# Optimization experiments

Measured on AMD Instinct MI355X. Metric: run time of the kernel, lower is better.

The kernel has to match this reference:

```python
import jax, jax.numpy as jnp
import numpy as np

N_NODES = 50000
NEG_SLOPE = 0.2  # PyG GATConv default LeakyReLU slope


def gat_conv(x, src, dst, W, att_src, att_dst, bias, heads, out_ch, concat):
    """PyG-style GATConv (dropout=0, add_self_loops omitted to match raw edge list usage).
    x: [N, in], W: [in, heads*out_ch], att_*: [1, heads, out_ch], bias: [heads*out_ch] or [out_ch].
    Messages flow src -> dst; softmax normalizes over incoming edges of each dst node."""
    N = x.shape[0]
    h = (x @ W).reshape(N, heads, out_ch)                      # [N,H,C]
    a_s = (h * att_src).sum(-1)                                # [N,H]
    a_d = (h * att_dst).sum(-1)                                # [N,H]
    e = jax.nn.leaky_relu(a_s[src] + a_d[dst], NEG_SLOPE)      # [E,H] per-edge logits
    m = jax.ops.segment_max(e, dst, num_segments=N)            # [N,H] stable softmax max
    p = jnp.exp(e - m[dst])                                    # [E,H]
    s = jax.ops.segment_sum(p, dst, num_segments=N)            # [N,H]
    alpha = p / (s[dst] + 1e-16)                               # [E,H] attention coeffs
    out = jax.ops.segment_sum(h[src] * alpha[:, :, None], dst, num_segments=N)  # [N,H,C]
    out = out.reshape(N, heads * out_ch) if concat else out.mean(axis=1)
    return out + bias


def setup_inputs() -> dict:
    key = jax.random.key(0)
    ks = jax.random.split(key, 10)
    in_ch, hid, heads, out_ch = 128, 32, 4, 64
    E = 800000
    x = jax.random.normal(ks[0], (N_NODES, in_ch), dtype=jnp.float32)
    edge_index = jax.random.randint(ks[1], (2, E), 0, N_NODES, dtype=jnp.int64)
    sc = 0.1
    return {
        "x": x,
        "edge_index": edge_index,
        "W1": jax.random.normal(ks[2], (in_ch, heads * hid), dtype=jnp.float32) * sc,
        "att_src1": jax.random.normal(ks[3], (1, heads, hid), dtype=jnp.float32) * sc,
        "att_dst1": jax.random.normal(ks[4], (1, heads, hid), dtype=jnp.float32) * sc,
        "b1": jnp.zeros((heads * hid,), dtype=jnp.float32),
        "W2": jax.random.normal(ks[5], (heads * hid, out_ch), dtype=jnp.float32) * sc,
        "att_src2": jax.random.normal(ks[6], (1, 1, out_ch), dtype=jnp.float32) * sc,
        "att_dst2": jax.random.normal(ks[7], (1, 1, out_ch), dtype=jnp.float32) * sc,
        "b2": jnp.zeros((out_ch,), dtype=jnp.float32),
    }


def reference(x, edge_index, W1, att_src1, att_dst1, b1, W2, att_src2, att_dst2, b2):
    src, dst = edge_index[0], edge_index[1]
    h = gat_conv(x, src, dst, W1, att_src1, att_dst1, b1, heads=4, out_ch=32, concat=True)
    h = jax.nn.elu(h)
    out = gat_conv(h, src, dst, W2, att_src2, att_dst2, b2, heads=1, out_ch=64, concat=False)
    return out
```

## Files before the change

kernel.cpp:

```cpp
#include <hip/hip_runtime.h>

#define N_NODES 50000
#define N_EDGES 800000
#define GEMM_BLKS ((N_NODES + 63) / 64)
#define FILL_BLKS 4096
#define RANGE 6250
#define EDGES_PER_BLK 1564
#define MAXDEG 64
#define AGG_BLKS (N_NODES / 4)

typedef __attribute__((ext_vector_type(8))) short bf16x8;
typedef __attribute__((ext_vector_type(4))) float f32x4;
typedef unsigned short u16;
typedef unsigned int u32;

__device__ __forceinline__ float lrelu(float x) { return x > 0.f ? x : 0.2f * x; }

__device__ __forceinline__ u16 f2bf(float f) {
    u32 u = __float_as_uint(f);
    return (u16)((u + 0x7FFFu + ((u >> 16) & 1u)) >> 16);
}
__device__ __forceinline__ float bflo(u32 w) { return __uint_as_float(w << 16); }
__device__ __forceinline__ float bfhi(u32 w) { return __uint_as_float(w & 0xFFFF0000u); }
__device__ __forceinline__ float elu(float x) { return x > 0.f ? x : __expf(x) - 1.f; }

__global__ __launch_bounds__(256) void k_prep(
    const float* __restrict__ W1, const float* __restrict__ as1v, const float* __restrict__ ad1v,
    const float* __restrict__ W2, const float* __restrict__ as2v, const float* __restrict__ ad2v,
    u16* __restrict__ Wt1, u16* __restrict__ Wt2, int* __restrict__ deg)
{
    int gid = blockIdx.x * 256 + threadIdx.x;
    for (int i = gid; i < N_NODES; i += 112 * 256) deg[i] = 0;
    if (gid < 144 * 128) {
        int n = gid >> 7, k = gid & 127;
        float v = 0.f;
        if (n < 128) v = W1[k * 128 + n];
        else if (n < 136) {
            int h = n - 128;
            const float* att = (h < 4) ? as1v : ad1v;
            int hh = h & 3;
            float s = 0.f;
            for (int c = 0; c < 32; ++c) s += W1[k * 128 + hh * 32 + c] * att[hh * 32 + c];
            v = s;
        }
        Wt1[n * 128 + k] = f2bf(v);
    } else {
        int g2 = gid - 144 * 128;
        if (g2 < 80 * 128) {
            int n = g2 >> 7, k = g2 & 127;
            float v = 0.f;
            if (n < 64) v = W2[k * 64 + n];
            else if (n == 64) { float s = 0.f; for (int c = 0; c < 64; ++c) s += W2[k * 64 + c] * as2v[c]; v = s; }
            else if (n == 65) { float s = 0.f; for (int c = 0; c < 64; ++c) s += W2[k * 64 + c] * ad2v[c]; v = s; }
            Wt2[n * 128 + k] = f2bf(v);
        }
    }
}

__global__ __launch_bounds__(256) void k_fill(
    const int* __restrict__ src, const int* __restrict__ dst,
    int* __restrict__ deg, u16* __restrict__ col16)
{
    const int g = blockIdx.x & 7;
    const int b = blockIdx.x >> 3;
    const int lo = g * RANGE;
    const int hi = min(lo + RANGE, N_NODES);
    const int e0 = b * EDGES_PER_BLK;
    const int e1 = min(e0 + EDGES_PER_BLK, N_EDGES);
    for (int e = e0 + threadIdx.x; e < e1; e += 256) {
        int v = dst[e];
        if (v >= lo && v < hi) {
            int pos = atomicAdd(&deg[v], 1);
            if (pos < MAXDEG) col16[v * MAXDEG + pos] = (u16)src[e];
        }
    }
}

__global__ __launch_bounds__(256) void k_gemm1(
    const float* __restrict__ x, const u16* __restrict__ Wt1,
    u16* __restrict__ hbf, float* __restrict__ as_, float* __restrict__ ad_)
{
    __shared__ u16 xs[64][136];
    __shared__ u16 ws[144][136];
    const int t = threadIdx.x;
    const int n0 = blockIdx.x * 64;
    #pragma unroll
    for (int it = 0; it < 8; ++it) {
        int idx = it * 256 + t;
        int row = idx >> 5, c4 = (idx & 31) * 4;
        int n = n0 + row;
        float4 xv = make_float4(0.f, 0.f, 0.f, 0.f);
        if (n < N_NODES) xv = *(const float4*)&x[(size_t)n * 128 + c4];
        uint2 pk;
        pk.x = (u32)f2bf(xv.x) | ((u32)f2bf(xv.y) << 16);
        pk.y = (u32)f2bf(xv.z) | ((u32)f2bf(xv.w) << 16);
        *(uint2*)&xs[row][c4] = pk;
    }
    #pragma unroll
    for (int it = 0; it < 9; ++it) {
        int idx = it * 256 + t;
        int row = idx >> 4, c8 = (idx & 15) * 8;
        *(uint4*)&ws[row][c8] = *(const uint4*)&Wt1[row * 128 + c8];
    }
    __syncthreads();
    const int l = t & 63, w = t >> 6;
    const int lm = l & 15, quad = l >> 4;
    f32x4 acc[9];
    #pragma unroll
    for (int nt = 0; nt < 9; ++nt) acc[nt] = (f32x4){0.f, 0.f, 0.f, 0.f};
    const u16* arow = &xs[w * 16 + lm][0];
    #pragma unroll
    for (int kc = 0; kc < 4; ++kc) {
        int k0 = kc * 32 + quad * 8;
        bf16x8 a = *(const bf16x8*)&arow[k0];
        #pragma unroll
        for (int nt = 0; nt < 9; ++nt) {
            bf16x8 b = *(const bf16x8*)&ws[nt * 16 + lm][k0];
            acc[nt] = __builtin_amdgcn_mfma_f32_16x16x32_bf16(a, b, acc[nt], 0, 0, 0);
        }
    }
    #pragma unroll
    for (int r = 0; r < 4; ++r) {
        int n = n0 + w * 16 + quad * 4 + r;
        if (n >= N_NODES) continue;
        #pragma unroll
        for (int nt = 0; nt < 8; ++nt)
            hbf[(size_t)n * 128 + nt * 16 + lm] = f2bf(acc[nt][r]);
        if (lm < 4)      as_[n * 4 + lm]     = acc[8][r];
        else if (lm < 8) ad_[n * 4 + lm - 4] = acc[8][r];
    }
}

__global__ __launch_bounds__(256) void k_agg1(
    const int* __restrict__ deg, const u16* __restrict__ col16,
    const float* __restrict__ as_, const float* __restrict__ ad_,
    const u32* __restrict__ h1u, const float* __restrict__ b1,
    u32* __restrict__ out1u)
{
    const int t = threadIdx.x;
    const int wv = t >> 6;
    const int l = t & 63;
    const int v = blockIdx.x * 4 + wv;
    const int c = l & 15;
    const int slot = l >> 4;
    const int hh = c >> 2;
    const int dg = min(deg[v], MAXDEG);
    const float adh = ad_[v * 4 + hh];
    const u16* cr = col16 + v * MAXDEG;
    float a[8] = {0.f, 0.f, 0.f, 0.f, 0.f, 0.f, 0.f, 0.f};
    float s = 0.f;
    for (int i0 = slot; i0 < dg; i0 += 8) {
        int i1 = i0 + 4;
        bool m1 = i1 < dg;
        int u0 = cr[i0];
        int u1 = cr[m1 ? i1 : i0];
        float p0 = __expf(lrelu(as_[u0 * 4 + hh] + adh));
        float p1 = m1 ? __expf(lrelu(as_[u1 * 4 + hh] + adh)) : 0.f;
        uint4 w0 = *(const uint4*)(h1u + (u0 << 6) + (c << 2));
        uint4 w1 = *(const uint4*)(h1u + (u1 << 6) + (c << 2));
        a[0] = fmaf(p0, bflo(w0.x), a[0]); a[1] = fmaf(p0, bfhi(w0.x), a[1]);
        a[2] = fmaf(p0, bflo(w0.y), a[2]); a[3] = fmaf(p0, bfhi(w0.y), a[3]);
        a[4] = fmaf(p0, bflo(w0.z), a[4]); a[5] = fmaf(p0, bfhi(w0.z), a[5]);
        a[6] = fmaf(p0, bflo(w0.w), a[6]); a[7] = fmaf(p0, bfhi(w0.w), a[7]);
        a[0] = fmaf(p1, bflo(w1.x), a[0]); a[1] = fmaf(p1, bfhi(w1.x), a[1]);
        a[2] = fmaf(p1, bflo(w1.y), a[2]); a[3] = fmaf(p1, bfhi(w1.y), a[3]);
        a[4] = fmaf(p1, bflo(w1.z), a[4]); a[5] = fmaf(p1, bfhi(w1.z), a[5]);
        a[6] = fmaf(p1, bflo(w1.w), a[6]); a[7] = fmaf(p1, bfhi(w1.w), a[7]);
        s += p0 + p1;
    }
    #pragma unroll
    for (int k = 0; k < 8; ++k) {
        a[k] += __shfl_xor(a[k], 16);
        a[k] += __shfl_xor(a[k], 32);
    }
    s += __shfl_xor(s, 16);
    s += __shfl_xor(s, 32);
    if (slot == 0) {
        float inv = 1.f / (s + 1e-16f);
        float4 b0 = *(const float4*)&b1[8 * c];
        float4 b4 = *(const float4*)&b1[8 * c + 4];
        float o0 = elu(a[0] * inv + b0.x);
        float o1 = elu(a[1] * inv + b0.y);
        float o2 = elu(a[2] * inv + b0.z);
        float o3 = elu(a[3] * inv + b0.w);
        float o4 = elu(a[4] * inv + b4.x);
        float o5 = elu(a[5] * inv + b4.y);
        float o6 = elu(a[6] * inv + b4.z);
        float o7 = elu(a[7] * inv + b4.w);
        uint4 pk;
        pk.x = (u32)f2bf(o0) | ((u32)f2bf(o1) << 16);
        pk.y = (u32)f2bf(o2) | ((u32)f2bf(o3) << 16);
        pk.z = (u32)f2bf(o4) | ((u32)f2bf(o5) << 16);
        pk.w = (u32)f2bf(o6) | ((u32)f2bf(o7) << 16);
        *(uint4*)(out1u + v * 64 + 4 * c) = pk;
    }
}

__global__ __launch_bounds__(256) void k_gemm2(
    const u16* __restrict__ xbf, const u16* __restrict__ Wt2,
    u16* __restrict__ hbf, float* __restrict__ as_, float* __restrict__ ad_)
{
    __shared__ u16 xs[64][136];
    __shared__ u16 ws[80][136];
    const int t = threadIdx.x;
    const int n0 = blockIdx.x * 64;
    #pragma unroll
    for (int it = 0; it < 4; ++it) {
        int idx = it * 256 + t;
        int row = idx >> 4, c8 = (idx & 15) * 8;
        int n = n0 + row;
        uint4 vv = make_uint4(0u, 0u, 0u, 0u);
        if (n < N_NODES) vv = *(const uint4*)&xbf[(size_t)n * 128 + c8];
        *(uint4*)&xs[row][c8] = vv;
    }
    #pragma unroll
    for (int it = 0; it < 5; ++it) {
        int idx = it * 256 + t;
        int row = idx >> 4, c8 = (idx & 15) * 8;
        *(uint4*)&ws[row][c8] = *(const uint4*)&Wt2[row * 128 + c8];
    }
    __syncthreads();
    const int l = t & 63, w = t >> 6;
    const int lm = l & 15, quad = l >> 4;
    f32x4 acc[5];
    #pragma unroll
    for (int nt = 0; nt < 5; ++nt) acc[nt] = (f32x4){0.f, 0.f, 0.f, 0.f};
    const u16* arow = &xs[w * 16 + lm][0];
    #pragma unroll
    for (int kc = 0; kc < 4; ++kc) {
        int k0 = kc * 32 + quad * 8;
        bf16x8 a = *(const bf16x8*)&arow[k0];
        #pragma unroll
        for (int nt = 0; nt < 5; ++nt) {
            bf16x8 b = *(const bf16x8*)&ws[nt * 16 + lm][k0];
            acc[nt] = __builtin_amdgcn_mfma_f32_16x16x32_bf16(a, b, acc[nt], 0, 0, 0);
        }
    }
    #pragma unroll
    for (int r = 0; r < 4; ++r) {
        int n = n0 + w * 16 + quad * 4 + r;
        if (n >= N_NODES) continue;
        #pragma unroll
        for (int nt = 0; nt < 4; ++nt)
            hbf[(size_t)n * 64 + nt * 16 + lm] = f2bf(acc[nt][r]);
        if (lm == 0)      as_[n] = acc[4][r];
        else if (lm == 1) ad_[n] = acc[4][r];
    }
}

__global__ __launch_bounds__(256) void k_agg2(
    const int* __restrict__ deg, const u16* __restrict__ col16,
    const float* __restrict__ as_, const float* __restrict__ ad_,
    const u32* __restrict__ h2u, const float* __restrict__ b2,
    float* __restrict__ out)
{
    const int t = threadIdx.x;
    const int wv = t >> 6;
    const int l = t & 63;
    const int v = blockIdx.x * 4 + wv;
    const int c = l & 7;
    const int slot = l >> 3;
    const int dg = min(deg[v], MAXDEG);
    const float adh = ad_[v];
    const u16* cr = col16 + v * MAXDEG;
    float a[8] = {0.f, 0.f, 0.f, 0.f, 0.f, 0.f, 0.f, 0.f};
    float s = 0.f;
    for (int i0 = slot; i0 < dg; i0 += 16) {
        int i1 = i0 + 8;
        bool m1 = i1 < dg;
        int u0 = cr[i0];
        int u1 = cr[m1 ? i1 : i0];
        float p0 = __expf(lrelu(as_[u0] + adh));
        float p1 = m1 ? __expf(lrelu(as_[u1] + adh)) : 0.f;
        uint4 w0 = *(const uint4*)(h2u + (u0 << 5) + (c << 2));
        uint4 w1 = *(const uint4*)(h2u + (u1 << 5) + (c << 2));
        a[0] = fmaf(p0, bflo(w0.x), a[0]); a[1] = fmaf(p0, bfhi(w0.x), a[1]);
        a[2] = fmaf(p0, bflo(w0.y), a[2]); a[3] = fmaf(p0, bfhi(w0.y), a[3]);
        a[4] = fmaf(p0, bflo(w0.z), a[4]); a[5] = fmaf(p0, bfhi(w0.z), a[5]);
        a[6] = fmaf(p0, bflo(w0.w), a[6]); a[7] = fmaf(p0, bfhi(w0.w), a[7]);
        a[0] = fmaf(p1, bflo(w1.x), a[0]); a[1] = fmaf(p1, bfhi(w1.x), a[1]);
        a[2] = fmaf(p1, bflo(w1.y), a[2]); a[3] = fmaf(p1, bfhi(w1.y), a[3]);
        a[4] = fmaf(p1, bflo(w1.z), a[4]); a[5] = fmaf(p1, bfhi(w1.z), a[5]);
        a[6] = fmaf(p1, bflo(w1.w), a[6]); a[7] = fmaf(p1, bfhi(w1.w), a[7]);
        s += p0 + p1;
    }
    #pragma unroll
    for (int k = 0; k < 8; ++k) {
        a[k] += __shfl_xor(a[k], 8);
        a[k] += __shfl_xor(a[k], 16);
        a[k] += __shfl_xor(a[k], 32);
    }
    s += __shfl_xor(s, 8);
    s += __shfl_xor(s, 16);
    s += __shfl_xor(s, 32);
    if (slot == 0) {
        float inv = 1.f / (s + 1e-16f);
        float4 b0 = *(const float4*)&b2[8 * c];
        float4 b4 = *(const float4*)&b2[8 * c + 4];
        float4 oa, ob;
        oa.x = a[0] * inv + b0.x;
        oa.y = a[1] * inv + b0.y;
        oa.z = a[2] * inv + b0.z;
        oa.w = a[3] * inv + b0.w;
        ob.x = a[4] * inv + b4.x;
        ob.y = a[5] * inv + b4.y;
        ob.z = a[6] * inv + b4.z;
        ob.w = a[7] * inv + b4.w;
        *(float4*)&out[(size_t)v * 64 + 8 * c]     = oa;
        *(float4*)&out[(size_t)v * 64 + 8 * c + 4] = ob;
    }
}

extern "C" void kernel_launch(void* const* d_in, const int* in_sizes, int n_in,
                              void* d_out, int out_size, void* d_ws, size_t ws_size,
                              hipStream_t stream)
{
    const float* x      = (const float*)d_in[0];
    const int*   ei     = (const int*)d_in[1];
    const float* W1     = (const float*)d_in[2];
    const float* att_s1 = (const float*)d_in[3];
    const float* att_d1 = (const float*)d_in[4];
    const float* b1     = (const float*)d_in[5];
    const float* W2     = (const float*)d_in[6];
    const float* att_s2 = (const float*)d_in[7];
    const float* att_d2 = (const float*)d_in[8];
    const float* b2     = (const float*)d_in[9];
    const int* src = ei;
    const int* dst = ei + N_EDGES;
    float* out = (float*)d_out;

    char* wsp = (char*)d_ws;
    u16* Wt1   = (u16*)wsp;  wsp += 144 * 128 * 2;
    u16* Wt2   = (u16*)wsp;  wsp += 80 * 128 * 2;
    u16* h1bf  = (u16*)wsp;  wsp += (size_t)N_NODES * 128 * 2;
    u16* o1bf  = (u16*)wsp;  wsp += (size_t)N_NODES * 128 * 2;
    u16* h2bf  = (u16*)wsp;  wsp += (size_t)N_NODES * 64 * 2;
    float* as1 = (float*)wsp; wsp += (size_t)N_NODES * 4 * 4;
    float* ad1 = (float*)wsp; wsp += (size_t)N_NODES * 4 * 4;
    float* as2 = (float*)wsp; wsp += (size_t)N_NODES * 4;
    float* ad2 = (float*)wsp; wsp += (size_t)N_NODES * 4;
    int* deg   = (int*)wsp;   wsp += (size_t)N_NODES * 4;
    u16* col16 = (u16*)wsp;  wsp += (size_t)N_NODES * MAXDEG * 2;

    k_prep<<<112, 256, 0, stream>>>(W1, att_s1, att_d1, W2, att_s2, att_d2, Wt1, Wt2, deg);
    k_fill<<<FILL_BLKS, 256, 0, stream>>>(src, dst, deg, col16);

    k_gemm1<<<GEMM_BLKS, 256, 0, stream>>>(x, Wt1, h1bf, as1, ad1);
    k_agg1<<<AGG_BLKS, 256, 0, stream>>>(deg, col16, as1, ad1, (const u32*)h1bf, b1, (u32*)o1bf);

    k_gemm2<<<GEMM_BLKS, 256, 0, stream>>>(o1bf, Wt2, h2bf, as2, ad2);
    k_agg2<<<AGG_BLKS, 256, 0, stream>>>(deg, col16, as2, ad2, (const u32*)h2bf, b2, out);
}
```

Before: 204.7 us.

## Fuse edge fill with first GEMM and load weights directly into registers

Merges the CSR fill kernel and the first projection GEMM into one launch, with block ranges split between the two roles, so the independent work can run concurrently and one launch is saved. Both GEMMs also drop the shared-memory staging of the weight matrix and load B fragments straight from global memory (L2-resident) into registers. This cuts LDS usage, which can raise occupancy, and removes a staging pass. The cost is higher register pressure and uncoalesced per-lane global loads for weights.

```diff
diff --git a/kernel.cpp b/kernel.cpp
--- a/kernel.cpp
+++ b/kernel.cpp
@@ -8,6 +8,7 @@
 #define EDGES_PER_BLK 1564
 #define MAXDEG 64
 #define AGG_BLKS (N_NODES / 4)
+#define FG1_BLKS (GEMM_BLKS + FILL_BLKS)
 
 typedef __attribute__((ext_vector_type(8))) short bf16x8;
 typedef __attribute__((ext_vector_type(4))) float f32x4;
@@ -57,32 +58,31 @@
     }
 }
 
-__global__ __launch_bounds__(256) void k_fill(
+__global__ __launch_bounds__(256) void k_fg1(
+    const float* __restrict__ x, const u16* __restrict__ Wt1,
+    u16* __restrict__ hbf, float* __restrict__ as_, float* __restrict__ ad_,
     const int* __restrict__ src, const int* __restrict__ dst,
     int* __restrict__ deg, u16* __restrict__ col16)
 {
-    const int g = blockIdx.x & 7;
-    const int b = blockIdx.x >> 3;
-    const int lo = g * RANGE;
-    const int hi = min(lo + RANGE, N_NODES);
-    const int e0 = b * EDGES_PER_BLK;
-    const int e1 = min(e0 + EDGES_PER_BLK, N_EDGES);
-    for (int e = e0 + threadIdx.x; e < e1; e += 256) {
-        int v = dst[e];
-        if (v >= lo && v < hi) {
-            int pos = atomicAdd(&deg[v], 1);
-            if (pos < MAXDEG) col16[v * MAXDEG + pos] = (u16)src[e];
+    const int t = threadIdx.x;
+    if (blockIdx.x >= GEMM_BLKS) {
+        const int bb = blockIdx.x - GEMM_BLKS;
+        const int g = bb & 7;
+        const int b = bb >> 3;
+        const int lo = g * RANGE;
+        const int hi = min(lo + RANGE, N_NODES);
+        const int e0 = b * EDGES_PER_BLK;
+        const int e1 = min(e0 + EDGES_PER_BLK, N_EDGES);
+        for (int e = e0 + t; e < e1; e += 256) {
+            int v = dst[e];
+            if (v >= lo && v < hi) {
+                int pos = atomicAdd(&deg[v], 1);
+                if (pos < MAXDEG) col16[v * MAXDEG + pos] = (u16)src[e];
+            }
         }
-    }
-}
-
-__global__ __launch_bounds__(256) void k_gemm1(
-    const float* __restrict__ x, const u16* __restrict__ Wt1,
-    u16* __restrict__ hbf, float* __restrict__ as_, float* __restrict__ ad_)
-{
+        return;
+    }
     __shared__ u16 xs[64][136];
-    __shared__ u16 ws[144][136];
-    const int t = threadIdx.x;
     const int n0 = blockIdx.x * 64;
     #pragma unroll
     for (int it = 0; it < 8; ++it) {
@@ -96,12 +96,6 @@
         pk.y = (u32)f2bf(xv.z) | ((u32)f2bf(xv.w) << 16);
         *(uint2*)&xs[row][c4] = pk;
     }
-    #pragma unroll
-    for (int it = 0; it < 9; ++it) {
-        int idx = it * 256 + t;
-        int row = idx >> 4, c8 = (idx & 15) * 8;
-        *(uint4*)&ws[row][c8] = *(const uint4*)&Wt1[row * 128 + c8];
-    }
     __syncthreads();
     const int l = t & 63, w = t >> 6;
     const int lm = l & 15, quad = l >> 4;
@@ -109,15 +103,35 @@
     #pragma unroll
     for (int nt = 0; nt < 9; ++nt) acc[nt] = (f32x4){0.f, 0.f, 0.f, 0.f};
     const u16* arow = &xs[w * 16 + lm][0];
-    #pragma unroll
-    for (int kc = 0; kc < 4; ++kc) {
-        int k0 = kc * 32 + quad * 8;
-        bf16x8 a = *(const bf16x8*)&arow[k0];
-        #pragma unroll
-        for (int nt = 0; nt < 9; ++nt) {
-            bf16x8 b = *(const bf16x8*)&ws[nt * 16 + lm][k0];
-            acc[nt] = __builtin_amdgcn_mfma_f32_16x16x32_bf16(a, b, acc[nt], 0, 0, 0);
-        }
+    const u16* brow = &Wt1[lm * 128 + quad * 8];
+    bf16x8 af[4];
+    #pragma unroll
+    for (int kc = 0; kc < 4; ++kc) af[kc] = *(const bf16x8*)&arow[kc * 32 + quad * 8];
+    {
+        bf16x8 bf[18];
+        #pragma unroll
+        for (int kc = 0; kc < 2; ++kc)
+            #pragma unroll
+            for (int nt = 0; nt < 9; ++nt)
+                bf[kc * 9 + nt] = *(const bf16x8*)&brow[nt * 2048 + kc * 32];
+        #pragma unroll
+        for (int kc = 0; kc < 2; ++kc)
+            #pragma unroll
+            for (int nt = 0; nt < 9; ++nt)
+                acc[nt] = __builtin_amdgcn_mfma_f32_16x16x32_bf16(af[kc], bf[kc * 9 + nt], acc[nt], 0, 0, 0);
+    }
+    {
+        bf16x8 bf[18];
+        #pragma unroll
+        for (int kc = 0; kc < 2; ++kc)
+            #pragma unroll
+            for (int nt = 0; nt < 9; ++nt)
+                bf[kc * 9 + nt] = *(const bf16x8*)&brow[nt * 2048 + (kc + 2) * 32];
+        #pragma unroll
+        for (int kc = 0; kc < 2; ++kc)
+            #pragma unroll
+            for (int nt = 0; nt < 9; ++nt)
+                acc[nt] = __builtin_amdgcn_mfma_f32_16x16x32_bf16(af[kc + 2], bf[kc * 9 + nt], acc[nt], 0, 0, 0);
     }
     #pragma unroll
     for (int r = 0; r < 4; ++r) {
@@ -201,7 +215,6 @@
     u16* __restrict__ hbf, float* __restrict__ as_, float* __restrict__ ad_)
 {
     __shared__ u16 xs[64][136];
-    __shared__ u16 ws[80][136];
     const int t = threadIdx.x;
     const int n0 = blockIdx.x * 64;
     #pragma unroll
@@ -213,12 +226,6 @@
         if (n < N_NODES) vv = *(const uint4*)&xbf[(size_t)n * 128 + c8];
         *(uint4*)&xs[row][c8] = vv;
     }
-    #pragma unroll
-    for (int it = 0; it < 5; ++it) {
-        int idx = it * 256 + t;
-        int row = idx >> 4, c8 = (idx & 15) * 8;
-        *(uint4*)&ws[row][c8] = *(const uint4*)&Wt2[row * 128 + c8];
-    }
     __syncthreads();
     const int l = t & 63, w = t >> 6;
     const int lm = l & 15, quad = l >> 4;
@@ -226,16 +233,21 @@
     #pragma unroll
     for (int nt = 0; nt < 5; ++nt) acc[nt] = (f32x4){0.f, 0.f, 0.f, 0.f};
     const u16* arow = &xs[w * 16 + lm][0];
-    #pragma unroll
-    for (int kc = 0; kc < 4; ++kc) {
-        int k0 = kc * 32 + quad * 8;
-        bf16x8 a = *(const bf16x8*)&arow[k0];
-        #pragma unroll
-        for (int nt = 0; nt < 5; ++nt) {
-            bf16x8 b = *(const bf16x8*)&ws[nt * 16 + lm][k0];
-            acc[nt] = __builtin_amdgcn_mfma_f32_16x16x32_bf16(a, b, acc[nt], 0, 0, 0);
-        }
-    }
+    const u16* brow = &Wt2[lm * 128 + quad * 8];
+    bf16x8 af[4];
+    #pragma unroll
+    for (int kc = 0; kc < 4; ++kc) af[kc] = *(const bf16x8*)&arow[kc * 32 + quad * 8];
+    bf16x8 bf[20];
+    #pragma unroll
+    for (int kc = 0; kc < 4; ++kc)
+        #pragma unroll
+        for (int nt = 0; nt < 5; ++nt)
+            bf[kc * 5 + nt] = *(const bf16x8*)&brow[nt * 2048 + kc * 32];
+    #pragma unroll
+    for (int kc = 0; kc < 4; ++kc)
+        #pragma unroll
+        for (int nt = 0; nt < 5; ++nt)
+            acc[nt] = __builtin_amdgcn_mfma_f32_16x16x32_bf16(af[kc], bf[kc * 5 + nt], acc[nt], 0, 0, 0);
     #pragma unroll
     for (int r = 0; r < 4; ++r) {
         int n = n0 + w * 16 + quad * 4 + r;
@@ -343,9 +355,9 @@
     u16* col16 = (u16*)wsp;  wsp += (size_t)N_NODES * MAXDEG * 2;
 
     k_prep<<<112, 256, 0, stream>>>(W1, att_s1, att_d1, W2, att_s2, att_d2, Wt1, Wt2, deg);
-    k_fill<<<FILL_BLKS, 256, 0, stream>>>(src, dst, deg, col16);
-
-    k_gemm1<<<GEMM_BLKS, 256, 0, stream>>>(x, Wt1, h1bf, as1, ad1);
+
+    k_fg1<<<FG1_BLKS, 256, 0, stream>>>(x, Wt1, h1bf, as1, ad1, src, dst, deg, col16);
+
     k_agg1<<<AGG_BLKS, 256, 0, stream>>>(deg, col16, as1, ad1, (const u32*)h1bf, b1, (u32*)o1bf);
 
     k_gemm2<<<GEMM_BLKS, 256, 0, stream>>>(o1bf, Wt2, h2bf, as2, ad2);
```

After: 215.4 us. 5.2% more time.

## Fuse layer-2 linear transform and attention scores into layer-1 aggregation kernel

Applied to the files above, without the earlier changes.

Removes the separate k_gemm2 kernel and the o1bf intermediate buffer. The ELU output is now kept in shared memory as fp32, and each wave computes the 64-wide W2 projection per node with scalar FMAs, then reduces the att_src/att_dst dot products with shuffles. This saves one launch plus a global round trip of the hidden activations. The cost is that MFMA is replaced by scalar FMAs reading bf16 weights from global/L2 for every node, which adds compute and load pressure to the aggregation kernel.

```diff
diff --git a/kernel.cpp b/kernel.cpp
--- a/kernel.cpp
+++ b/kernel.cpp
@@ -22,12 +22,13 @@
 }
 __device__ __forceinline__ float bflo(u32 w) { return __uint_as_float(w << 16); }
 __device__ __forceinline__ float bfhi(u32 w) { return __uint_as_float(w & 0xFFFF0000u); }
+__device__ __forceinline__ float bfu(u16 w) { return __uint_as_float((u32)w << 16); }
 __device__ __forceinline__ float elu(float x) { return x > 0.f ? x : __expf(x) - 1.f; }
 
 __global__ __launch_bounds__(256) void k_prep(
     const float* __restrict__ W1, const float* __restrict__ as1v, const float* __restrict__ ad1v,
-    const float* __restrict__ W2, const float* __restrict__ as2v, const float* __restrict__ ad2v,
-    u16* __restrict__ Wt1, u16* __restrict__ Wt2, int* __restrict__ deg)
+    const float* __restrict__ W2,
+    u16* __restrict__ Wt1, u16* __restrict__ Wt2T, int* __restrict__ deg)
 {
     int gid = blockIdx.x * 256 + threadIdx.x;
     for (int i = gid; i < N_NODES; i += 112 * 256) deg[i] = 0;
@@ -46,13 +47,9 @@
         Wt1[n * 128 + k] = f2bf(v);
     } else {
         int g2 = gid - 144 * 128;
-        if (g2 < 80 * 128) {
+        if (g2 < 64 * 128) {
             int n = g2 >> 7, k = g2 & 127;
-            float v = 0.f;
-            if (n < 64) v = W2[k * 64 + n];
-            else if (n == 64) { float s = 0.f; for (int c = 0; c < 64; ++c) s += W2[k * 64 + c] * as2v[c]; v = s; }
-            else if (n == 65) { float s = 0.f; for (int c = 0; c < 64; ++c) s += W2[k * 64 + c] * ad2v[c]; v = s; }
-            Wt2[n * 128 + k] = f2bf(v);
+            Wt2T[k * 64 + n] = f2bf(W2[k * 64 + n]);
         }
     }
 }
@@ -135,8 +132,10 @@
     const int* __restrict__ deg, const u16* __restrict__ col16,
     const float* __restrict__ as_, const float* __restrict__ ad_,
     const u32* __restrict__ h1u, const float* __restrict__ b1,
-    u32* __restrict__ out1u)
-{
+    const u16* __restrict__ Wt2T, const float* __restrict__ atts2, const float* __restrict__ attd2,
+    u16* __restrict__ h2bf, float* __restrict__ as2, float* __restrict__ ad2)
+{
+    __shared__ float hv[4][128];
     const int t = threadIdx.x;
     const int wv = t >> 6;
     const int l = t & 63;
@@ -179,73 +178,30 @@
         float inv = 1.f / (s + 1e-16f);
         float4 b0 = *(const float4*)&b1[8 * c];
         float4 b4 = *(const float4*)&b1[8 * c + 4];
-        float o0 = elu(a[0] * inv + b0.x);
-        float o1 = elu(a[1] * inv + b0.y);
-        float o2 = elu(a[2] * inv + b0.z);
-        float o3 = elu(a[3] * inv + b0.w);
-        float o4 = elu(a[4] * inv + b4.x);
-        float o5 = elu(a[5] * inv + b4.y);
-        float o6 = elu(a[6] * inv + b4.z);
-        float o7 = elu(a[7] * inv + b4.w);
-        uint4 pk;
-        pk.x = (u32)f2bf(o0) | ((u32)f2bf(o1) << 16);
-        pk.y = (u32)f2bf(o2) | ((u32)f2bf(o3) << 16);
-        pk.z = (u32)f2bf(o4) | ((u32)f2bf(o5) << 16);
-        pk.w = (u32)f2bf(o6) | ((u32)f2bf(o7) << 16);
-        *(uint4*)(out1u + v * 64 + 4 * c) = pk;
-    }
-}
-
-__global__ __launch_bounds__(256) void k_gemm2(
-    const u16* __restrict__ xbf, const u16* __restrict__ Wt2,
-    u16* __restrict__ hbf, float* __restrict__ as_, float* __restrict__ ad_)
-{
-    __shared__ u16 xs[64][136];
-    __shared__ u16 ws[80][136];
-    const int t = threadIdx.x;
-    const int n0 = blockIdx.x * 64;
-    #pragma unroll
-    for (int it = 0; it < 4; ++it) {
-        int idx = it * 256 + t;
-        int row = idx >> 4, c8 = (idx & 15) * 8;
-        int n = n0 + row;
-        uint4 vv = make_uint4(0u, 0u, 0u, 0u);
-        if (n < N_NODES) vv = *(const uint4*)&xbf[(size_t)n * 128 + c8];
-        *(uint4*)&xs[row][c8] = vv;
-    }
-    #pragma unroll
-    for (int it = 0; it < 5; ++it) {
-        int idx = it * 256 + t;
-        int row = idx >> 4, c8 = (idx & 15) * 8;
-        *(uint4*)&ws[row][c8] = *(const uint4*)&Wt2[row * 128 + c8];
+        float4 t0, t1;
+        t0.x = elu(a[0] * inv + b0.x);
+        t0.y = elu(a[1] * inv + b0.y);
+        t0.z = elu(a[2] * inv + b0.z);
+        t0.w = elu(a[3] * inv + b0.w);
+        t1.x = elu(a[4] * inv + b4.x);
+        t1.y = elu(a[5] * inv + b4.y);
+        t1.z = elu(a[6] * inv + b4.z);
+        t1.w = elu(a[7] * inv + b4.w);
+        *(float4*)&hv[wv][8 * c]     = t0;
+        *(float4*)&hv[wv][8 * c + 4] = t1;
     }
     __syncthreads();
-    const int l = t & 63, w = t >> 6;
-    const int lm = l & 15, quad = l >> 4;
-    f32x4 acc[5];
-    #pragma unroll
-    for (int nt = 0; nt < 5; ++nt) acc[nt] = (f32x4){0.f, 0.f, 0.f, 0.f};
-    const u16* arow = &xs[w * 16 + lm][0];
-    #pragma unroll
-    for (int kc = 0; kc < 4; ++kc) {
-        int k0 = kc * 32 + quad * 8;
-        bf16x8 a = *(const bf16x8*)&arow[k0];
-        #pragma unroll
-        for (int nt = 0; nt < 5; ++nt) {
-            bf16x8 b = *(const bf16x8*)&ws[nt * 16 + lm][k0];
-            acc[nt] = __builtin_amdgcn_mfma_f32_16x16x32_bf16(a, b, acc[nt], 0, 0, 0);
-        }
-    }
-    #pragma unroll
-    for (int r = 0; r < 4; ++r) {
-        int n = n0 + w * 16 + quad * 4 + r;
-        if (n >= N_NODES) continue;
-        #pragma unroll
-        for (int nt = 0; nt < 4; ++nt)
-            hbf[(size_t)n * 64 + nt * 16 + lm] = f2bf(acc[nt][r]);
-        if (lm == 0)      as_[n] = acc[4][r];
-        else if (lm == 1) ad_[n] = acc[4][r];
-    }
+    float acc = 0.f;
+    const float* hrow = hv[wv];
+    #pragma unroll 8
+    for (int k = 0; k < 128; ++k)
+        acc = fmaf(hrow[k], bfu(Wt2T[k * 64 + l]), acc);
+    float sa = acc * atts2[l];
+    float sd = acc * attd2[l];
+    #pragma unroll
+    for (int m = 1; m < 64; m <<= 1) { sa += __shfl_xor(sa, m); sd += __shfl_xor(sd, m); }
+    h2bf[(size_t)v * 64 + l] = f2bf(acc);
+    if (l == 0) { as2[v] = sa; ad2[v] = sd; }
 }
 
 __global__ __launch_bounds__(256) void k_agg2(
@@ -331,9 +287,8 @@
 
     char* wsp = (char*)d_ws;
     u16* Wt1   = (u16*)wsp;  wsp += 144 * 128 * 2;
-    u16* Wt2   = (u16*)wsp;  wsp += 80 * 128 * 2;
+    u16* Wt2T  = (u16*)wsp;  wsp += 128 * 64 * 2;
     u16* h1bf  = (u16*)wsp;  wsp += (size_t)N_NODES * 128 * 2;
-    u16* o1bf  = (u16*)wsp;  wsp += (size_t)N_NODES * 128 * 2;
     u16* h2bf  = (u16*)wsp;  wsp += (size_t)N_NODES * 64 * 2;
     float* as1 = (float*)wsp; wsp += (size_t)N_NODES * 4 * 4;
     float* ad1 = (float*)wsp; wsp += (size_t)N_NODES * 4 * 4;
@@ -342,12 +297,13 @@
     int* deg   = (int*)wsp;   wsp += (size_t)N_NODES * 4;
     u16* col16 = (u16*)wsp;  wsp += (size_t)N_NODES * MAXDEG * 2;
 
-    k_prep<<<112, 256, 0, stream>>>(W1, att_s1, att_d1, W2, att_s2, att_d2, Wt1, Wt2, deg);
+    k_prep<<<112, 256, 0, stream>>>(W1, att_s1, att_d1, W2, Wt1, Wt2T, deg);
     k_fill<<<FILL_BLKS, 256, 0, stream>>>(src, dst, deg, col16);
 
     k_gemm1<<<GEMM_BLKS, 256, 0, stream>>>(x, Wt1, h1bf, as1, ad1);
-    k_agg1<<<AGG_BLKS, 256, 0, stream>>>(deg, col16, as1, ad1, (const u32*)h1bf, b1, (u32*)o1bf);
-
-    k_gemm2<<<GEMM_BLKS, 256, 0, stream>>>(o1bf, Wt2, h2bf, as2, ad2);
+
+    k_agg1<<<AGG_BLKS, 256, 0, stream>>>(deg, col16, as1, ad1, (const u32*)h1bf, b1,
+                                         Wt2T, att_s2, att_d2, h2bf, as2, ad2);
+
     k_agg2<<<AGG_BLKS, 256, 0, stream>>>(deg, col16, as2, ad2, (const u32*)h2bf, b2, out);
 }
```

After: 239.3 us. 1.17x slower.
